# Optimization experiments

Hardware: AMD Instinct MI355X
Metric: run time of the kernel (lower is better)

## Reference

```python
import jax, jax.numpy as jnp
import numpy as np

B, S, H, V, NH, FF, M, NL = 16, 512, 256, 8000, 4, 512, 64, 2
BETA, THR, ALPHA = 0.9, 1.0, 2.0  # snn.Leaky defaults: beta=0.9, threshold=1.0, ATan surrogate alpha=2


@jax.custom_vjp
def spike(u):
    return (u > 0).astype(u.dtype)

def _spike_fwd(u):
    return (u > 0).astype(u.dtype), u

def _spike_bwd(u, g):
    # snntorch ATan surrogate gradient
    return (g * (ALPHA / 2.0) / (1.0 + (jnp.pi * u * ALPHA / 2.0) ** 2),)

spike.defvjp(_spike_fwd, _spike_bwd)


def layer_norm(x, g, b):
    m = x.mean(-1, keepdims=True)
    v = ((x - m) ** 2).mean(-1, keepdims=True)
    return (x - m) / jnp.sqrt(v + 1e-5) * g + b


def mha(x, wqkv, bqkv, wo, bo):
    Bx, Sx, Hx = x.shape
    hd = Hx // NH
    qkv = x @ wqkv.T + bqkv
    q, k, v = jnp.split(qkv, 3, axis=-1)
    sp = lambda t: t.reshape(Bx, Sx, NH, hd).transpose(0, 2, 1, 3)
    q, k, v = sp(q), sp(k), sp(v)
    att = jax.nn.softmax(jnp.einsum('bhqd,bhkd->bhqk', q, k) / (float(hd) ** 0.5), axis=-1)
    o = jnp.einsum('bhqk,bhkd->bhqd', att, v).transpose(0, 2, 1, 3).reshape(Bx, Sx, Hx)
    return o @ wo.T + bo


def spiking_worker(x, w, b):
    # batched projection for all timesteps, then a single-pass LIF scan
    proj = x @ w.T + b  # [B,S,H]

    def step(mem, xt):
        reset = spike(mem - THR)              # spike detected from previous membrane
        mem = BETA * mem + xt - reset * THR   # subtract-reset mechanism
        return mem, spike(mem - THR)

    mem0 = jnp.zeros((x.shape[0], x.shape[2]), x.dtype)
    _, spks = jax.lax.scan(step, mem0, jnp.swapaxes(proj, 0, 1))
    return jnp.swapaxes(spks, 0, 1)  # [B,S,H]


def _forward(input_ids, embed, pos, qkv_w, qkv_b, out_w, out_b, ln1_g, ln1_b,
             ff1_w, ff1_b, ff2_w, ff2_b, ln2_g, ln2_b,
             log_w, log_b, mat_w, mat_b, conv_w, conv_b,
             read_w, read_b, memory, head_w, head_b):
    x = embed[input_ids] + pos[:, :input_ids.shape[1], :]
    for i in range(NL):  # post-norm TransformerEncoderLayer x2, gelu, eval mode
        x = layer_norm(x + mha(x, qkv_w[i], qkv_b[i], out_w[i], out_b[i]), ln1_g[i], ln1_b[i])
        h = jax.nn.gelu(x @ ff1_w[i].T + ff1_b[i], approximate=False) @ ff2_w[i].T + ff2_b[i]
        x = layer_norm(x + h, ln2_g[i], ln2_b[i])
    plan = x
    logico = spiking_worker(plan, log_w, log_b)
    matem = spiking_worker(plan, mat_w, mat_b)
    ling = jax.lax.conv_general_dilated(
        jnp.swapaxes(plan, 1, 2), conv_w, (1,), [(1, 1)],
        dimension_numbers=('NCH', 'OIH', 'NCH')) + conv_b[None, :, None]
    ling = jnp.swapaxes(ling, 1, 2)
    combined = jnp.concatenate([logico, matem, ling, plan], axis=-1)  # [B,S,4H]
    plan_mean = plan.mean(axis=1)                                      # [B,H]
    read_weights = jax.nn.softmax(plan_mean @ read_w.T + read_b, axis=-1)
    memory_read = read_weights @ memory                                # [B,H]
    logits = combined @ head_w.T + head_b                              # [B,S,V]
    return logits, memory_read


def setup_inputs() -> dict:
    key = jax.random.key(0)
    ks = iter(jax.random.split(key, 32))
    sc = 0.02
    rn = lambda shape, s=sc: jax.random.normal(next(ks), shape, jnp.float32) * s
    inp = {
        'input_ids': jax.random.randint(next(ks), (B, S), 0, V),
        'embed': rn((V, H), 1.0),
        'pos': rn((1, 512, H), 1.0),
        'qkv_w': rn((NL, 3 * H, H)), 'qkv_b': rn((NL, 3 * H)),
        'out_w': rn((NL, H, H)), 'out_b': rn((NL, H)),
        'ln1_g': jnp.ones((NL, H), jnp.float32), 'ln1_b': jnp.zeros((NL, H), jnp.float32),
        'ff1_w': rn((NL, FF, H)), 'ff1_b': rn((NL, FF)),
        'ff2_w': rn((NL, H, FF)), 'ff2_b': rn((NL, H)),
        'ln2_g': jnp.ones((NL, H), jnp.float32), 'ln2_b': jnp.zeros((NL, H), jnp.float32),
        'log_w': rn((H, H)), 'log_b': rn((H,)),
        'mat_w': rn((H, H)), 'mat_b': rn((H,)),
        'conv_w': rn((H, H, 3)), 'conv_b': rn((H,)),
        'read_w': rn((M, H)), 'read_b': rn((M,)),
        'memory': rn((M, H), 1.0),
        'head_w': rn((V, 4 * H)), 'head_b': rn((V,)),
    }
    return inp


def reference(input_ids, embed, pos, qkv_w, qkv_b, out_w, out_b, ln1_g, ln1_b,
              ff1_w, ff1_b, ff2_w, ff2_b, ln2_g, ln2_b,
              log_w, log_b, mat_w, mat_b, conv_w, conv_b,
              read_w, read_b, memory, head_w, head_b):
    return _forward(input_ids, embed, pos, qkv_w, qkv_b, out_w, out_b, ln1_g, ln1_b,
                    ff1_w, ff1_b, ff2_w, ff2_b, ln2_g, ln2_b,
                    log_w, log_b, mat_w, mat_b, conv_w, conv_b,
                    read_w, read_b, memory, head_w, head_b)
```

## Files before the change

### kernel.cpp

```cpp
#include <hip/hip_runtime.h>
#include <hip/hip_bf16.h>

constexpr int Bc = 16, Sc = 512, Hc = 256, Vc = 8000, NHc = 4, HDc = 64;
constexpr int FFc = 512, Mc = 64;
constexpr int ROWS = Bc * Sc;
constexpr int CH = 4 * Hc;
constexpr int NT2 = CH / 32;

typedef __attribute__((ext_vector_type(4))) float f32x4v;
typedef __attribute__((ext_vector_type(8))) short short8v;
typedef __attribute__((ext_vector_type(4))) short short4v;
typedef __hip_bfloat16 bf16;

__device__ inline void split3(float x, bf16& h, bf16& m, bf16& l) {
    h = __float2bfloat16(x);
    const float r = x - __bfloat162float(h);
    m = __float2bfloat16(r);
    const float r2 = r - __bfloat162float(m);
    l = __float2bfloat16(r2);
}

__device__ __forceinline__ void split_range(const float* __restrict__ in,
                                            bf16* __restrict__ h, bf16* __restrict__ m,
                                            bf16* __restrict__ l, int blk, int t) {
    const size_t i = ((size_t)blk * 256 + t) * 4;
    const float4 v = *(const float4*)&in[i];
    split3(v.x, h[i + 0], m[i + 0], l[i + 0]);
    split3(v.y, h[i + 1], m[i + 1], l[i + 1]);
    split3(v.z, h[i + 2], m[i + 2], l[i + 2]);
    split3(v.w, h[i + 3], m[i + 3], l[i + 3]);
}

__global__ __launch_bounds__(256) void k_prep(
    const float* __restrict__ qkv_w, const float* __restrict__ out_w,
    const float* __restrict__ ff1_w, const float* __restrict__ ff2_w,
    const float* __restrict__ log_w, const float* __restrict__ mat_w,
    const float* __restrict__ conv_w, const float* __restrict__ head_w,
    const float* __restrict__ log_b, const float* __restrict__ mat_b,
    bf16* qkvwh, bf16* qkvwm, bf16* qkvwl,
    bf16* outwh, bf16* outwm, bf16* outwl,
    bf16* ff1wh, bf16* ff1wm, bf16* ff1wl,
    bf16* ff2wh, bf16* ff2wm, bf16* ff2wl,
    bf16* lmwh, bf16* lmwm, bf16* lmwl,
    bf16* w2h, bf16* w2m, bf16* w2l,
    bf16* hwb, float* lmb) {
    const int blk = blockIdx.x;
    const int t = threadIdx.x;
    if (blk < 384) {
        split_range(qkv_w, qkvwh, qkvwm, qkvwl, blk, t);
    } else if (blk < 512) {
        split_range(out_w, outwh, outwm, outwl, blk - 384, t);
    } else if (blk < 768) {
        split_range(ff1_w, ff1wh, ff1wm, ff1wl, blk - 512, t);
    } else if (blk < 1024) {
        split_range(ff2_w, ff2wh, ff2wm, ff2wl, blk - 768, t);
    } else if (blk < 1088) {
        split_range(log_w, lmwh, lmwm, lmwl, blk - 1024, t);
    } else if (blk < 1152) {
        split_range(mat_w, lmwh + 65536, lmwm + 65536, lmwl + 65536, blk - 1088, t);
    } else if (blk < 1920) {
        const int idx = (blk - 1152) * 256 + t;
        const int o = idx / 768, rem = idx % 768;
        const int k = rem >> 8, i = rem & 255;
        split3(conv_w[(size_t)o * 768 + i * 3 + k], w2h[idx], w2m[idx], w2l[idx]);
    } else if (blk < 9920) {
        const size_t i = ((size_t)(blk - 1920) * 256 + t) * 4;
        const float4 v = *(const float4*)&head_w[i];
        bf16 b0 = __float2bfloat16(v.x), b1 = __float2bfloat16(v.y);
        bf16 b2 = __float2bfloat16(v.z), b3 = __float2bfloat16(v.w);
        short4v sv;
        sv[0] = *(const short*)&b0; sv[1] = *(const short*)&b1;
        sv[2] = *(const short*)&b2; sv[3] = *(const short*)&b3;
        *(short4v*)(hwb + i) = sv;
    } else {
        lmb[t] = log_b[t];
        lmb[256 + t] = mat_b[t];
    }
}

__global__ __launch_bounds__(256) void k_embed(const int* __restrict__ ids,
                                               const float* __restrict__ emb,
                                               const float* __restrict__ pos,
                                               float* __restrict__ x,
                                               bf16* __restrict__ xh, bf16* __restrict__ xm,
                                               bf16* __restrict__ xl) {
    const int r = blockIdx.x;
    const int h = threadIdx.x;
    const int s = r & (Sc - 1);
    const int id = ids[r];
    const float v = emb[(size_t)id * Hc + h] + pos[(size_t)s * Hc + h];
    const size_t o = (size_t)r * Hc + h;
    x[o] = v;
    split3(v, xh[o], xm[o], xl[o]);
}

template <int EPI, int OUTS, int BN>
__global__ __launch_bounds__(256) void k_bg3(
    const bf16* __restrict__ Ah, const bf16* __restrict__ Am, const bf16* __restrict__ Al,
    const bf16* __restrict__ Bh, const bf16* __restrict__ Bm, const bf16* __restrict__ Bl,
    const float* __restrict__ bias, float* __restrict__ C,
    bf16* __restrict__ Oh, bf16* __restrict__ Om, bf16* __restrict__ Ol,
    int K, int lda, int ldb, int ldc,
    long zA2, long zA1, long zB2, long zB1, long zC2, long zC1) {
    constexpr int NF = BN / 32;
    __shared__ bf16 As[3][128 * 32];
    __shared__ bf16 Bs[3][BN * 32];
    const int z = blockIdx.z, z2 = z >> 2, z1 = z & 3;
    const size_t aoff = (size_t)z2 * zA2 + (size_t)z1 * zA1;
    const size_t boff = (size_t)z2 * zB2 + (size_t)z1 * zB1;
    const size_t coff = (size_t)z2 * zC2 + (size_t)z1 * zC1;
    const int t = threadIdx.x;
    const int tm = blockIdx.x * 128, tn = blockIdx.y * BN;
    const int w = t >> 6, l = t & 63;
    const int wr = w >> 1, wc = w & 1;
    const bf16* Ap[3] = {Ah, Am, Al};
    const bf16* Bp[3] = {Bh, Bm, Bl};
    f32x4v acc[4][NF];
    const f32x4v zero = {0.f, 0.f, 0.f, 0.f};
#pragma unroll
    for (int i = 0; i < 4; ++i)
#pragma unroll
        for (int j = 0; j < NF; ++j) acc[i][j] = zero;

    for (int kt = 0; kt < K; kt += 32) {
#pragma unroll
        for (int p = 0; p < 3; ++p) {
#pragma unroll
            for (int j = 0; j < 2; ++j) {
                const int c = j * 256 + t;
                const int row = c >> 2, kc = c & 3;
                const int skc = kc ^ ((row >> 1) & 3);
                const bf16* ga = Ap[p] + aoff + (size_t)(tm + row) * lda + kt + skc * 8;
                __builtin_amdgcn_global_load_lds((const __attribute__((address_space(1))) void*)ga,
                                                 (__attribute__((address_space(3))) void*)(&As[p][0] + c * 8),
                                                 16, 0, 0);
            }
            if (BN == 128) {
#pragma unroll
                for (int j = 0; j < 2; ++j) {
                    const int c = j * 256 + t;
                    const int row = c >> 2, kc = c & 3;
                    const int skc = kc ^ ((row >> 1) & 3);
                    const bf16* gb = Bp[p] + boff + (size_t)(tn + row) * ldb + kt + skc * 8;
                    __builtin_amdgcn_global_load_lds((const __attribute__((address_space(1))) void*)gb,
                                                     (__attribute__((address_space(3))) void*)(&Bs[p][0] + c * 8),
                                                     16, 0, 0);
                }
            } else {
                const int c = t;
                const int row = c >> 2, kc = c & 3;
                const int skc = kc ^ ((row >> 1) & 3);
                const bf16* gb = Bp[p] + boff + (size_t)(tn + row) * ldb + kt + skc * 8;
                __builtin_amdgcn_global_load_lds((const __attribute__((address_space(1))) void*)gb,
                                                 (__attribute__((address_space(3))) void*)(&Bs[p][0] + c * 8),
                                                 16, 0, 0);
            }
        }
        __syncthreads();
        const int lr = l & 15, lkc = l >> 4;
        short8v af[3][4], bfr[3][NF];
#pragma unroll
        for (int p = 0; p < 3; ++p)
#pragma unroll
            for (int m = 0; m < 4; ++m) {
                const int row = wr * 64 + m * 16 + lr;
                const int sc = lkc ^ ((row >> 1) & 3);
                af[p][m] = *(const short8v*)(&As[p][0] + row * 32 + sc * 8);
            }
#pragma unroll
        for (int p = 0; p < 3; ++p)
#pragma unroll
            for (int n = 0; n < NF; ++n) {
                const int row = wc * (BN / 2) + n * 16 + lr;
                const int sc = lkc ^ ((row >> 1) & 3);
                bfr[p][n] = *(const short8v*)(&Bs[p][0] + row * 32 + sc * 8);
            }
#pragma unroll
        for (int m = 0; m < 4; ++m)
#pragma unroll
            for (int n = 0; n < NF; ++n)
                acc[m][n] = __builtin_amdgcn_mfma_f32_16x16x32_bf16(af[0][m], bfr[0][n], acc[m][n], 0, 0, 0);
#pragma unroll
        for (int m = 0; m < 4; ++m)
#pragma unroll
            for (int n = 0; n < NF; ++n)
                acc[m][n] = __builtin_amdgcn_mfma_f32_16x16x32_bf16(af[0][m], bfr[1][n], acc[m][n], 0, 0, 0);
#pragma unroll
        for (int m = 0; m < 4; ++m)
#pragma unroll
            for (int n = 0; n < NF; ++n)
                acc[m][n] = __builtin_amdgcn_mfma_f32_16x16x32_bf16(af[1][m], bfr[0][n], acc[m][n], 0, 0, 0);
#pragma unroll
        for (int m = 0; m < 4; ++m)
#pragma unroll
            for (int n = 0; n < NF; ++n)
                acc[m][n] = __builtin_amdgcn_mfma_f32_16x16x32_bf16(af[0][m], bfr[2][n], acc[m][n], 0, 0, 0);
#pragma unroll
        for (int m = 0; m < 4; ++m)
#pragma unroll
            for (int n = 0; n < NF; ++n)
                acc[m][n] = __builtin_amdgcn_mfma_f32_16x16x32_bf16(af[2][m], bfr[0][n], acc[m][n], 0, 0, 0);
#pragma unroll
        for (int m = 0; m < 4; ++m)
#pragma unroll
            for (int n = 0; n < NF; ++n)
                acc[m][n] = __builtin_amdgcn_mfma_f32_16x16x32_bf16(af[1][m], bfr[1][n], acc[m][n], 0, 0, 0);
        __syncthreads();
    }
    const int lr = l & 15, lq = (l >> 4) * 4;
#pragma unroll
    for (int n = 0; n < NF; ++n) {
        const int col = tn + wc * (BN / 2) + n * 16 + lr;
        const float bv = (EPI == 0 || EPI == 1) ? bias[col] : 0.0f;
#pragma unroll
        for (int m = 0; m < 4; ++m) {
            const int rbase = tm + wr * 64 + m * 16 + lq;
#pragma unroll
            for (int j = 0; j < 4; ++j) {
                float v = acc[m][n][j];
                if (EPI == 0) v += bv;
                if (EPI == 1) { v += bv; v = 0.5f * v * (1.0f + erff(v / 1.41421356237309515f)); }
                const size_t o = coff + (size_t)(rbase + j) * ldc + col;
                if (OUTS == 0) C[o] = v;
                else if (OUTS == 3) ((bf16*)C)[o] = __float2bfloat16(v);
                else split3(v, Oh[o], Om[o], Ol[o]);
            }
        }
    }
}

__global__ __launch_bounds__(256) void k_vt(const bf16* __restrict__ qh,
                                            const bf16* __restrict__ qm,
                                            const bf16* __restrict__ ql,
                                            bf16* __restrict__ vh, bf16* __restrict__ vm,
                                            bf16* __restrict__ vl) {
    __shared__ bf16 tile[64][72];
    const int sblk = blockIdx.x;
    const int z = blockIdx.y;
    const int b = z >> 2, h = z & 3;
    const int t = threadIdx.x;
    const int sr = t >> 2, c16 = (t & 3) * 16;
    const bf16* qp[3] = {qh, qm, ql};
    bf16* vp[3] = {vh, vm, vl};
    for (int p = 0; p < 3; ++p) {
        const bf16* src = qp[p] + (size_t)(b * Sc + sblk * 64 + sr) * 768 + 512 + h * 64 + c16;
        *(short8v*)&tile[sr][c16] = *(const short8v*)src;
        *(short8v*)&tile[sr][c16 + 8] = *(const short8v*)(src + 8);
        __syncthreads();
        bf16 out[16];
#pragma unroll
        for (int i = 0; i < 16; ++i) out[i] = tile[c16 + i][sr];
        bf16* dst = vp[p] + (size_t)(z * 64 + sr) * Sc + sblk * 64 + c16;
        *(short8v*)dst = *(short8v*)&out[0];
        *(short8v*)(dst + 8) = *(short8v*)&out[8];
        __syncthreads();
    }
}

#define S_PASS(QA, KB)                                                                     \
    _Pragma("unroll") for (int m = 0; m < 2; ++m) _Pragma("unroll") for (int ks = 0; ks < 2; ++ks) \
        sa[m] = __builtin_amdgcn_mfma_f32_16x16x32_bf16(QA[m][ks], KB[ks], sa[m], 0, 0, 0);
#define PV_PASS(PA, VB)                                                                    \
    _Pragma("unroll") for (int m = 0; m < 2; ++m) _Pragma("unroll") for (int ks = 0; ks < 2; ++ks) \
        oa[m] = __builtin_amdgcn_mfma_f32_16x16x32_bf16(PA[m][ks], VB[ks], oa[m], 0, 0, 0);

__global__ __launch_bounds__(512) void k_attn(
    const bf16* __restrict__ qph, const bf16* __restrict__ qpm, const bf16* __restrict__ qpl,
    const bf16* __restrict__ vth, const bf16* __restrict__ vtm, const bf16* __restrict__ vtl,
    bf16* __restrict__ oh, bf16* __restrict__ om, bf16* __restrict__ ol) {
    extern __shared__ char smem[];
    float* S = (float*)smem;
    bf16* KV0 = (bf16*)(smem + 131072);
    bf16* KV1 = KV0 + 4096;
    bf16* KV2 = KV1 + 4096;
    const int qc = blockIdx.x, z = blockIdx.y;
    const int b = z >> 2, hh = z & 3;
    const int t = threadIdx.x;
    const int w = t >> 6, lane = t & 63;
    const int lr = lane & 15, lkc = lane >> 4;
    const int qg = w >> 2, kg = w & 3;
    const int r8 = t >> 3, c8 = t & 7;
    const f32x4v zero = {0.f, 0.f, 0.f, 0.f};

    short8v qf0[2][2], qf1[2][2], qf2[2][2];
#pragma unroll
    for (int m = 0; m < 2; ++m)
#pragma unroll
        for (int ks = 0; ks < 2; ++ks) {
            const size_t rbase = (size_t)(b * 512 + qc * 64 + qg * 32 + m * 16 + lr) * 768 + hh * 64 + ks * 32 + lkc * 8;
            qf0[m][ks] = *(const short8v*)(qph + rbase);
            qf1[m][ks] = *(const short8v*)(qpm + rbase);
            qf2[m][ks] = *(const short8v*)(qpl + rbase);
        }

    {
        const size_t srow = (size_t)(b * 512 + 0 * 64 + r8) * 768 + 256 + hh * 64 + (c8 ^ (r8 & 7)) * 8;
        __builtin_amdgcn_global_load_lds((const __attribute__((address_space(1))) void*)(qph + srow),
                                         (__attribute__((address_space(3))) void*)(KV0 + r8 * 64 + c8 * 8), 16, 0, 0);
        __builtin_amdgcn_global_load_lds((const __attribute__((address_space(1))) void*)(qpm + srow),
                                         (__attribute__((address_space(3))) void*)(KV1 + r8 * 64 + c8 * 8), 16, 0, 0);
        __builtin_amdgcn_global_load_lds((const __attribute__((address_space(1))) void*)(qpl + srow),
                                         (__attribute__((address_space(3))) void*)(KV2 + r8 * 64 + c8 * 8), 16, 0, 0);
    }

    for (int kv = 0; kv < 8; ++kv) {
        __syncthreads();
        short8v kb0[2], kb1[2], kb2[2];
#pragma unroll
        for (int ks = 0; ks < 2; ++ks) {
            const int row = kg * 16 + lr;
            const int sc = (ks * 4 + lkc) ^ (row & 7);
            kb0[ks] = *(const short8v*)(KV0 + row * 64 + sc * 8);
            kb1[ks] = *(const short8v*)(KV1 + row * 64 + sc * 8);
            kb2[ks] = *(const short8v*)(KV2 + row * 64 + sc * 8);
        }
        __syncthreads();
        if (kv < 7) {
            const size_t srow = (size_t)(b * 512 + (kv + 1) * 64 + r8) * 768 + 256 + hh * 64 + (c8 ^ (r8 & 7)) * 8;
            __builtin_amdgcn_global_load_lds((const __attribute__((address_space(1))) void*)(qph + srow),
                                             (__attribute__((address_space(3))) void*)(KV0 + r8 * 64 + c8 * 8), 16, 0, 0);
            __builtin_amdgcn_global_load_lds((const __attribute__((address_space(1))) void*)(qpm + srow),
                                             (__attribute__((address_space(3))) void*)(KV1 + r8 * 64 + c8 * 8), 16, 0, 0);
            __builtin_amdgcn_global_load_lds((const __attribute__((address_space(1))) void*)(qpl + srow),
                                             (__attribute__((address_space(3))) void*)(KV2 + r8 * 64 + c8 * 8), 16, 0, 0);
        } else {
            const size_t srow = (size_t)(z * 64 + r8) * 512 + 0 * 64 + (c8 ^ (r8 & 7)) * 8;
            __builtin_amdgcn_global_load_lds((const __attribute__((address_space(1))) void*)(vth + srow),
                                             (__attribute__((address_space(3))) void*)(KV0 + r8 * 64 + c8 * 8), 16, 0, 0);
            __builtin_amdgcn_global_load_lds((const __attribute__((address_space(1))) void*)(vtm + srow),
                                             (__attribute__((address_space(3))) void*)(KV1 + r8 * 64 + c8 * 8), 16, 0, 0);
            __builtin_amdgcn_global_load_lds((const __attribute__((address_space(1))) void*)(vtl + srow),
                                             (__attribute__((address_space(3))) void*)(KV2 + r8 * 64 + c8 * 8), 16, 0, 0);
        }
        f32x4v sa[2] = {zero, zero};
        S_PASS(qf0, kb0) S_PASS(qf0, kb1) S_PASS(qf1, kb0)
        S_PASS(qf0, kb2) S_PASS(qf2, kb0) S_PASS(qf1, kb1)
#pragma unroll
        for (int m = 0; m < 2; ++m)
#pragma unroll
            for (int j = 0; j < 4; ++j) {
                const int row = qg * 32 + m * 16 + (lane >> 4) * 4 + j;
                const int col = kv * 64 + kg * 16 + lr;
                const int chunk = (col >> 2) ^ (row & 7);
                *(float*)((char*)S + row * 2048 + chunk * 16 + (col & 3) * 4) = sa[m][j] * 0.125f;
            }
    }
    __syncthreads();

    for (int r = 0; r < 8; ++r) {
        const int row = w * 8 + r;
        char* rowp = (char*)S + row * 2048;
        const int sw = row & 7;
        float4 x0 = *(float4*)(rowp + ((2 * lane) ^ sw) * 16);
        float4 x1 = *(float4*)(rowp + ((2 * lane + 1) ^ sw) * 16);
        float mx = fmaxf(fmaxf(fmaxf(x0.x, x0.y), fmaxf(x0.z, x0.w)),
                         fmaxf(fmaxf(x1.x, x1.y), fmaxf(x1.z, x1.w)));
#pragma unroll
        for (int d = 1; d < 64; d <<= 1) mx = fmaxf(mx, __shfl_xor(mx, d));
        const float e0 = expf(x0.x - mx), e1 = expf(x0.y - mx), e2 = expf(x0.z - mx), e3 = expf(x0.w - mx);
        const float e4 = expf(x1.x - mx), e5 = expf(x1.y - mx), e6 = expf(x1.z - mx), e7 = expf(x1.w - mx);
        float sm = ((e0 + e1) + (e2 + e3)) + ((e4 + e5) + (e6 + e7));
#pragma unroll
        for (int d = 1; d < 64; d <<= 1) sm += __shfl_xor(sm, d);
        x0.x = e0 / sm; x0.y = e1 / sm; x0.z = e2 / sm; x0.w = e3 / sm;
        x1.x = e4 / sm; x1.y = e5 / sm; x1.z = e6 / sm; x1.w = e7 / sm;
        *(float4*)(rowp + ((2 * lane) ^ sw) * 16) = x0;
        *(float4*)(rowp + ((2 * lane + 1) ^ sw) * 16) = x1;
    }
    __syncthreads();

    f32x4v oa[2] = {zero, zero};
    for (int kv = 0; kv < 8; ++kv) {
        if (kv > 0) __syncthreads();
        short8v vb0[2], vb1[2], vb2[2];
#pragma unroll
        for (int ks = 0; ks < 2; ++ks) {
            const int rowd = kg * 16 + lr;
            const int sc = (ks * 4 + lkc) ^ (rowd & 7);
            vb0[ks] = *(const short8v*)(KV0 + rowd * 64 + sc * 8);
            vb1[ks] = *(const short8v*)(KV1 + rowd * 64 + sc * 8);
            vb2[ks] = *(const short8v*)(KV2 + rowd * 64 + sc * 8);
        }
        __syncthreads();
        if (kv < 7) {
            const size_t srow = (size_t)(z * 64 + r8) * 512 + (kv + 1) * 64 + (c8 ^ (r8 & 7)) * 8;
            __builtin_amdgcn_global_load_lds((const __attribute__((address_space(1))) void*)(vth + srow),
                                             (__attribute__((address_space(3))) void*)(KV0 + r8 * 64 + c8 * 8), 16, 0, 0);
            __builtin_amdgcn_global_load_lds((const __attribute__((address_space(1))) void*)(vtm + srow),
                                             (__attribute__((address_space(3))) void*)(KV1 + r8 * 64 + c8 * 8), 16, 0, 0);
            __builtin_amdgcn_global_load_lds((const __attribute__((address_space(1))) void*)(vtl + srow),
                                             (__attribute__((address_space(3))) void*)(KV2 + r8 * 64 + c8 * 8), 16, 0, 0);
        }
        short8v pah[2][2], pam[2][2], pal[2][2];
#pragma unroll
        for (int m = 0; m < 2; ++m)
#pragma unroll
            for (int ks = 0; ks < 2; ++ks) {
                const int row = qg * 32 + m * 16 + lr;
                const int c0 = kv * 16 + ks * 8 + lkc * 2;
                char* rp = (char*)S + row * 2048;
                const float4 y0 = *(const float4*)(rp + (c0 ^ (row & 7)) * 16);
                const float4 y1 = *(const float4*)(rp + ((c0 + 1) ^ (row & 7)) * 16);
                const float yy[8] = {y0.x, y0.y, y0.z, y0.w, y1.x, y1.y, y1.z, y1.w};
                short8v hv, mv, lv;
#pragma unroll
                for (int i = 0; i < 8; ++i) {
                    bf16 a, bq, c;
                    split3(yy[i], a, bq, c);
                    hv[i] = *(const short*)&a; mv[i] = *(const short*)&bq; lv[i] = *(const short*)&c;
                }
                pah[m][ks] = hv; pam[m][ks] = mv; pal[m][ks] = lv;
            }
        PV_PASS(pah, vb0) PV_PASS(pah, vb1) PV_PASS(pam, vb0)
        PV_PASS(pah, vb2) PV_PASS(pal, vb0) PV_PASS(pam, vb1)
    }
#pragma unroll
    for (int m = 0; m < 2; ++m)
#pragma unroll
        for (int j = 0; j < 4; ++j) {
            const int grow = b * 512 + qc * 64 + qg * 32 + m * 16 + (lane >> 4) * 4 + j;
            const int col = hh * 64 + kg * 16 + lr;
            const size_t o = (size_t)grow * 256 + col;
            split3(oa[m][j], oh[o], om[o], ol[o]);
        }
}

__global__ __launch_bounds__(256) void k_add_ln(float* __restrict__ x,
                                                const float* __restrict__ res,
                                                const float* __restrict__ g,
                                                const float* __restrict__ b,
                                                bf16* __restrict__ xh, bf16* __restrict__ xm,
                                                bf16* __restrict__ xl,
                                                bf16* __restrict__ comb) {
    const int w = threadIdx.x >> 6, lane = threadIdx.x & 63;
    const size_t row = (size_t)blockIdx.x * 4 + w;
    float v[4];
#pragma unroll
    for (int j = 0; j < 4; ++j) {
        const int e = lane + j * 64;
        v[j] = x[row * Hc + e] + res[row * Hc + e];
    }
    float a = v[0] + v[2];
    float bb = v[1] + v[3];
    float c = a + bb;
#pragma unroll
    for (int d = 32; d >= 1; d >>= 1) c += __shfl_xor(c, d);
    const float mean = c * (1.0f / 256.0f);
    float dd[4], sq[4];
#pragma unroll
    for (int j = 0; j < 4; ++j) {
        dd[j] = v[j] - mean;
        sq[j] = dd[j] * dd[j];
        asm volatile("" : "+v"(sq[j]));
    }
    float a2 = sq[0] + sq[2];
    float b2 = sq[1] + sq[3];
    float c2 = a2 + b2;
#pragma unroll
    for (int d = 32; d >= 1; d >>= 1) c2 += __shfl_xor(c2, d);
    const float var = c2 * (1.0f / 256.0f);
    const float rstd = sqrtf(var + 1e-5f);
#pragma unroll
    for (int j = 0; j < 4; ++j) {
        const int e = lane + j * 64;
        const float out = dd[j] / rstd * g[e] + b[e];
        const size_t o = row * Hc + e;
        x[o] = out;
        split3(out, xh[o], xm[o], xl[o]);
        if (comb != nullptr) comb[row * CH + 768 + e] = __float2bfloat16(out);
    }
}

__global__ __launch_bounds__(256) void k_lif2(const float* __restrict__ lm,
                                              bf16* __restrict__ comb) {
    const int b = blockIdx.x;
    const int half = blockIdx.y;
    const int h = threadIdx.x;
    const float* p = lm + (size_t)b * Sc * 512 + half * 256 + h;
    bf16* o = comb + (size_t)b * Sc * CH + half * 256 + h;
    float mem = 0.0f;
    for (int s0 = 0; s0 < Sc; s0 += 8) {
        float xs[8];
#pragma unroll
        for (int q = 0; q < 8; ++q) xs[q] = p[(size_t)(s0 + q) * 512];
#pragma unroll
        for (int q = 0; q < 8; ++q) {
            const float reset = (mem > 1.0f) ? 1.0f : 0.0f;
            float t1 = 0.9f * mem;
            asm volatile("" : "+v"(t1));
            float t2 = t1 + xs[q];
            asm volatile("" : "+v"(t2));
            mem = t2 - reset;
            o[(size_t)(s0 + q) * CH] = __float2bfloat16((mem > 1.0f) ? 1.0f : 0.0f);
        }
    }
}

__global__ __launch_bounds__(256) void k_aext3(const bf16* __restrict__ xh,
                                               const bf16* __restrict__ xm,
                                               const bf16* __restrict__ xl,
                                               bf16* __restrict__ aeh, bf16* __restrict__ aem,
                                               bf16* __restrict__ ael) {
    const int idx = blockIdx.x * 256 + threadIdx.x;
    const int row = idx / 192, c4 = idx % 192;
    const int c = c4 * 4;
    const int k = c >> 8, i = c & 255;
    const int b = row >> 9, s = row & 511;
    const int ss = s + k - 1;
    const size_t dst = (size_t)row * 768 + c;
    if (ss >= 0 && ss < Sc) {
        const size_t src = (size_t)(b * Sc + ss) * Hc + i;
        *(short4v*)(aeh + dst) = *(const short4v*)(xh + src);
        *(short4v*)(aem + dst) = *(const short4v*)(xm + src);
        *(short4v*)(ael + dst) = *(const short4v*)(xl + src);
    } else {
        const short4v z = {0, 0, 0, 0};
        *(short4v*)(aeh + dst) = z;
        *(short4v*)(aem + dst) = z;
        *(short4v*)(ael + dst) = z;
    }
}

__device__ __forceinline__ void stageA32(const bf16* __restrict__ g, int rbase,
                                         bf16* lbase, int kt, int t) {
#pragma unroll
    for (int q = 0; q < 2; ++q) {
        const int f = q * 256 + t;
        const int rowt = f >> 2, chunk = f & 3;
        const int sch = chunk ^ ((rowt >> 1) & 3);
        const bf16* gp = g + (size_t)(rbase + rowt) * CH + kt * 32 + sch * 8;
        __builtin_amdgcn_global_load_lds((const __attribute__((address_space(1))) void*)gp,
                                         (__attribute__((address_space(3))) void*)(lbase + rowt * 32 + chunk * 8),
                                         16, 0, 0);
    }
}
__device__ __forceinline__ void stageB32(const bf16* __restrict__ g, int rbase, int rmax,
                                         bf16* lbase, int kt, int t) {
#pragma unroll
    for (int q = 0; q < 4; ++q) {
        const int f = q * 256 + t;
        const int rowt = f >> 2, chunk = f & 3;
        const int sch = chunk ^ ((rowt >> 1) & 3);
        int grow = rbase + rowt;
        if (grow > rmax) grow = rmax;
        const bf16* gp = g + (size_t)grow * CH + kt * 32 + sch * 8;
        __builtin_amdgcn_global_load_lds((const __attribute__((address_space(1))) void*)gp,
                                         (__attribute__((address_space(3))) void*)(lbase + rowt * 32 + chunk * 8),
                                         16, 0, 0);
    }
}

__global__ __launch_bounds__(256, 2) void k_head8(const bf16* __restrict__ Abf,
                                                  const bf16* __restrict__ Bbf,
                                                  const float* __restrict__ bias,
                                                  float* __restrict__ C) {
    __shared__ bf16 LA[2][128 * 32];
    __shared__ bf16 LB[2][256 * 32];
    const int t = threadIdx.x;
    const int w = t >> 6, lane = t & 63;
    const int wn = w;
    const int tm = blockIdx.x * 128, tn = blockIdx.y * 256;
    const int lr = lane & 15, lkc = lane >> 4;

    f32x4v acc[8][4];
    const f32x4v zero = {0.f, 0.f, 0.f, 0.f};
#pragma unroll
    for (int m = 0; m < 8; ++m)
#pragma unroll
        for (int n = 0; n < 4; ++n) acc[m][n] = zero;

    stageA32(Abf, tm, LA[0], 0, t);
    stageB32(Bbf, tn, Vc - 1, LB[0], 0, t);
    stageA32(Abf, tm, LA[1], 1, t);
    asm volatile("s_waitcnt vmcnt(2)" ::: "memory");
    __builtin_amdgcn_s_barrier();
    __builtin_amdgcn_sched_barrier(0);

    for (int kt = 0; kt < NT2; ++kt) {
        bf16* la = LA[kt & 1];
        bf16* lb = LB[kt & 1];
        bf16* lbN = LB[(kt + 1) & 1];
        short8v a[8], b[4];
#pragma unroll
        for (int m = 0; m < 8; ++m) {
            const int row = m * 16 + lr;
            const int sc = lkc ^ ((row >> 1) & 3);
            a[m] = *(const short8v*)(la + row * 32 + sc * 8);
        }
#pragma unroll
        for (int n = 0; n < 4; ++n) {
            const int row = wn * 64 + n * 16 + lr;
            const int sc = lkc ^ ((row >> 1) & 3);
            b[n] = *(const short8v*)(lb + row * 32 + sc * 8);
        }
        if (kt + 1 < NT2) stageB32(Bbf, tn, Vc - 1, lbN, kt + 1, t);
        __builtin_amdgcn_s_barrier();
        __builtin_amdgcn_sched_barrier(0);
        __builtin_amdgcn_s_setprio(1);
#pragma unroll
        for (int m = 0; m < 8; ++m)
#pragma unroll
            for (int n = 0; n < 2; ++n)
                acc[m][n] = __builtin_amdgcn_mfma_f32_16x16x32_bf16(a[m], b[n], acc[m][n], 0, 0, 0);
        __builtin_amdgcn_s_setprio(0);
        __builtin_amdgcn_s_barrier();
        __builtin_amdgcn_sched_barrier(0);
        if (kt + 2 < NT2) stageA32(Abf, tm, la, kt + 2, t);
        __builtin_amdgcn_s_setprio(1);
#pragma unroll
        for (int m = 0; m < 8; ++m)
#pragma unroll
            for (int n = 2; n < 4; ++n)
                acc[m][n] = __builtin_amdgcn_mfma_f32_16x16x32_bf16(a[m], b[n], acc[m][n], 0, 0, 0);
        __builtin_amdgcn_s_setprio(0);
        if (kt + 2 < NT2) asm volatile("s_waitcnt vmcnt(2)" ::: "memory");
        else              asm volatile("s_waitcnt vmcnt(0)" ::: "memory");
        __builtin_amdgcn_s_barrier();
        __builtin_amdgcn_sched_barrier(0);
    }
    const int lq = (lane >> 4) * 4;
#pragma unroll
    for (int n = 0; n < 4; ++n) {
        const int col = tn + wn * 64 + n * 16 + lr;
        if (col >= Vc) continue;
        const float bv = bias[col];
#pragma unroll
        for (int m = 0; m < 8; ++m) {
            const int rbase = tm + m * 16 + lq;
#pragma unroll
            for (int j = 0; j < 4; ++j)
                C[(size_t)(rbase + j) * Vc + col] = acc[m][n][j] + bv;
        }
    }
}

__global__ __launch_bounds__(256) void k_pmean(const float* __restrict__ plan, float* __restrict__ pm2) {
    const int b = blockIdx.x, c = blockIdx.y;
    const int h = threadIdx.x;
    const float* p = plan + ((size_t)(b * Sc + c * 64)) * Hc + h;
    float s = 0.0f;
    for (int i = 0; i < 64; ++i) s += p[(size_t)i * Hc];
    pm2[((size_t)b * 8 + c) * Hc + h] = s;
}

__global__ __launch_bounds__(256) void k_memread(const float* __restrict__ pm2,
                                                 const float* __restrict__ rw,
                                                 const float* __restrict__ rb,
                                                 const float* __restrict__ memm,
                                                 float* __restrict__ out) {
    const int b = blockIdx.x;
    const int t = threadIdx.x;
    __shared__ float pms[256];
    __shared__ float lg[64];
    __shared__ float sm[64];
    float v = 0.0f;
    for (int c = 0; c < 8; ++c) v += pm2[((size_t)b * 8 + c) * Hc + t];
    pms[t] = v * (1.0f / 512.0f);
    __syncthreads();
    if (t < 64) {
        float s = rb[t];
        const float* wrow = rw + (size_t)t * Hc;
        for (int i = 0; i < Hc; ++i) s = fmaf(wrow[i], pms[i], s);
        lg[t] = s;
    }
    __syncthreads();
    if (t == 0) {
        float mx = lg[0];
        for (int i = 1; i < 64; ++i) mx = fmaxf(mx, lg[i]);
        float ssum = 0.0f;
        for (int i = 0; i < 64; ++i) { const float e = expf(lg[i] - mx); sm[i] = e; ssum += e; }
        for (int i = 0; i < 64; ++i) sm[i] /= ssum;
    }
    __syncthreads();
    float s = 0.0f;
    for (int m = 0; m < 64; ++m) s = fmaf(sm[m], memm[(size_t)m * Hc + t], s);
    out[(size_t)b * Hc + t] = s;
}

extern "C" void kernel_launch(void* const* d_in, const int* in_sizes, int n_in,
                              void* d_out, int out_size, void* d_ws, size_t ws_size,
                              hipStream_t stream) {
    const int*   ids    = (const int*)  d_in[0];
    const float* embed  = (const float*)d_in[1];
    const float* pos    = (const float*)d_in[2];
    const float* qkv_w  = (const float*)d_in[3];
    const float* qkv_b  = (const float*)d_in[4];
    const float* out_w  = (const float*)d_in[5];
    const float* out_b  = (const float*)d_in[6];
    const float* ln1_g  = (const float*)d_in[7];
    const float* ln1_b  = (const float*)d_in[8];
    const float* ff1_w  = (const float*)d_in[9];
    const float* ff1_b  = (const float*)d_in[10];
    const float* ff2_w  = (const float*)d_in[11];
    const float* ff2_b  = (const float*)d_in[12];
    const float* ln2_g  = (const float*)d_in[13];
    const float* ln2_b  = (const float*)d_in[14];
    const float* log_w  = (const float*)d_in[15];
    const float* log_b  = (const float*)d_in[16];
    const float* mat_w  = (const float*)d_in[17];
    const float* mat_b  = (const float*)d_in[18];
    const float* conv_w = (const float*)d_in[19];
    const float* conv_b = (const float*)d_in[20];
    const float* read_w = (const float*)d_in[21];
    const float* read_b = (const float*)d_in[22];
    const float* memory = (const float*)d_in[23];
    const float* head_w = (const float*)d_in[24];
    const float* head_b = (const float*)d_in[25];

    char* wsb = (char*)d_ws;
    const size_t MB = 1ull << 20;
    float* X    = (float*)(wsb + 0);
    bf16*  XH   = (bf16*)(wsb + 8 * MB);
    bf16*  XM   = (bf16*)(wsb + 12 * MB);
    bf16*  XL   = (bf16*)(wsb + 16 * MB);
    float* RES  = (float*)(wsb + 20 * MB);
    bf16*  QPH  = (bf16*)(wsb + 28 * MB);
    bf16*  QPM  = (bf16*)(wsb + 40 * MB);
    bf16*  QPL  = (bf16*)(wsb + 52 * MB);
    bf16*  OH   = (bf16*)(wsb + 64 * MB);
    bf16*  OM   = (bf16*)(wsb + 68 * MB);
    bf16*  OL   = (bf16*)(wsb + 72 * MB);
    bf16*  VTH  = (bf16*)(wsb + 76 * MB);
    bf16*  VTM  = (bf16*)(wsb + 80 * MB);
    bf16*  VTL  = (bf16*)(wsb + 84 * MB);
    bf16*  H1H  = (bf16*)(wsb + 88 * MB);
    bf16*  H1M  = (bf16*)(wsb + 96 * MB);
    bf16*  H1L  = (bf16*)(wsb + 104 * MB);
    float* LOGMAT = (float*)(wsb + 76 * MB);
    bf16*  AEH  = (bf16*)(wsb + 92 * MB);
    bf16*  AEM  = (bf16*)(wsb + 104 * MB);
    bf16*  AEL  = (bf16*)(wsb + 116 * MB);
    bf16*  COMB = (bf16*)(wsb + 128 * MB);
    bf16*  HWB  = (bf16*)(wsb + 144 * MB);
    bf16*  WP   = (bf16*)(wsb + 160 * MB);
    float* PM2  = (float*)(wsb + 64 * MB);

    float* logits = (float*)d_out;
    float* mread  = logits + (size_t)ROWS * Vc;

    bf16* qkvwh = WP;             bf16* qkvwm = qkvwh + 393216; bf16* qkvwl = qkvwm + 393216;
    bf16* outwh = qkvwl + 393216; bf16* outwm = outwh + 131072; bf16* outwl = outwm + 131072;
    bf16* ff1wh = outwl + 131072; bf16* ff1wm = ff1wh + 262144; bf16* ff1wl = ff1wm + 262144;
    bf16* ff2wh = ff1wl + 262144; bf16* ff2wm = ff2wh + 262144; bf16* ff2wl = ff2wm + 262144;
    bf16* lmwh  = ff2wl + 262144; bf16* lmwm  = lmwh + 131072;  bf16* lmwl  = lmwm + 131072;
    bf16* w2h   = lmwl + 131072;  bf16* w2m   = w2h + 196608;   bf16* w2l   = w2m + 196608;
    float* LMB  = (float*)(w2l + 196608);

    hipFuncSetAttribute((const void*)k_attn, hipFuncAttributeMaxDynamicSharedMemorySize, 155648);

    k_prep<<<dim3(9921), 256, 0, stream>>>(
        qkv_w, out_w, ff1_w, ff2_w, log_w, mat_w, conv_w, head_w, log_b, mat_b,
        qkvwh, qkvwm, qkvwl, outwh, outwm, outwl, ff1wh, ff1wm, ff1wl,
        ff2wh, ff2wm, ff2wl, lmwh, lmwm, lmwl, w2h, w2m, w2l, HWB, LMB);

    k_embed<<<dim3(ROWS), 256, 0, stream>>>(ids, embed, pos, X, XH, XM, XL);
    for (int l = 0; l < 2; ++l) {
        k_bg3<0, 1, 128><<<dim3(64, 6, 1), 256, 0, stream>>>(
            XH, XM, XL,
            qkvwh + (size_t)l * 196608, qkvwm + (size_t)l * 196608, qkvwl + (size_t)l * 196608,
            qkv_b + l * 768, nullptr, QPH, QPM, QPL,
            256, 256, 256, 768, 0, 0, 0, 0, 0, 0);
        k_vt<<<dim3(8, 64), 256, 0, stream>>>(QPH, QPM, QPL, VTH, VTM, VTL);
        k_attn<<<dim3(8, 64), 512, 155648, stream>>>(QPH, QPM, QPL, VTH, VTM, VTL, OH, OM, OL);
        k_bg3<0, 0, 64><<<dim3(64, 4, 1), 256, 0, stream>>>(
            OH, OM, OL,
            outwh + (size_t)l * 65536, outwm + (size_t)l * 65536, outwl + (size_t)l * 65536,
            out_b + l * 256, RES, nullptr, nullptr, nullptr,
            256, 256, 256, 256, 0, 0, 0, 0, 0, 0);
        k_add_ln<<<dim3(ROWS / 4), 256, 0, stream>>>(X, RES, ln1_g + l * 256, ln1_b + l * 256,
                                                     XH, XM, XL, nullptr);
        k_bg3<1, 1, 128><<<dim3(64, 4, 1), 256, 0, stream>>>(
            XH, XM, XL,
            ff1wh + (size_t)l * 131072, ff1wm + (size_t)l * 131072, ff1wl + (size_t)l * 131072,
            ff1_b + l * 512, nullptr, H1H, H1M, H1L,
            256, 256, 256, 512, 0, 0, 0, 0, 0, 0);
        k_bg3<0, 0, 64><<<dim3(64, 4, 1), 256, 0, stream>>>(
            H1H, H1M, H1L,
            ff2wh + (size_t)l * 131072, ff2wm + (size_t)l * 131072, ff2wl + (size_t)l * 131072,
            ff2_b + l * 256, RES, nullptr, nullptr, nullptr,
            512, 512, 512, 256, 0, 0, 0, 0, 0, 0);
        k_add_ln<<<dim3(ROWS / 4), 256, 0, stream>>>(X, RES, ln2_g + l * 256, ln2_b + l * 256,
                                                     XH, XM, XL, (l == 1) ? COMB : nullptr);
    }
    k_bg3<0, 0, 128><<<dim3(64, 4, 1), 256, 0, stream>>>(
        XH, XM, XL, lmwh, lmwm, lmwl, LMB, LOGMAT, nullptr, nullptr, nullptr,
        256, 256, 256, 512, 0, 0, 0, 0, 0, 0);
    k_aext3<<<dim3(6144), 256, 0, stream>>>(XH, XM, XL, AEH, AEM, AEL);
    k_lif2<<<dim3(Bc, 2), 256, 0, stream>>>(LOGMAT, COMB);
    k_bg3<0, 3, 64><<<dim3(64, 4, 1), 256, 0, stream>>>(
        AEH, AEM, AEL, w2h, w2m, w2l, conv_b, (float*)(COMB + 512), nullptr, nullptr, nullptr,
        768, 768, 768, CH, 0, 0, 0, 0, 0, 0);
    k_head8<<<dim3(64, 32), 256, 0, stream>>>(COMB, HWB, head_b, logits);
    k_pmean<<<dim3(Bc, 8), 256, 0, stream>>>(X, PM2);
    k_memread<<<dim3(Bc), 256, 0, stream>>>(PM2, read_w, read_b, memory, mread);
}
```

Before: 720.8 us.

## Fuse conv im2col into GEMM loads, vectorize embed, batch vt transposes

Removes the separate im2col kernel (k_aext3) that materialized a 3x-expanded activation in three bf16 planes. The conv GEMM now computes shifted source addresses on the fly and points out-of-range halo rows at a small zero buffer. This saves roughly 36MB of writes plus the matching re-reads. The embed kernel is vectorized to four rows per block using float4/short4 accesses, and k_vt loads all three precision planes before a single sync instead of syncing per plane. The address computation in the GEMM load loop adds some integer work per load.

```diff
diff --git a/kernel.cpp b/kernel.cpp
--- a/kernel.cpp
+++ b/kernel.cpp
@@ -43,7 +43,7 @@
     bf16* ff2wh, bf16* ff2wm, bf16* ff2wl,
     bf16* lmwh, bf16* lmwm, bf16* lmwl,
     bf16* w2h, bf16* w2m, bf16* w2l,
-    bf16* hwb, float* lmb) {
+    bf16* hwb, float* lmb, bf16* zb) {
     const int blk = blockIdx.x;
     const int t = threadIdx.x;
     if (blk < 384) {
@@ -75,6 +75,7 @@
     } else {
         lmb[t] = log_b[t];
         lmb[256 + t] = mat_b[t];
+        if (t < 64) ((short*)zb)[t] = 0;
     }
 }
 
@@ -84,24 +85,37 @@
                                                float* __restrict__ x,
                                                bf16* __restrict__ xh, bf16* __restrict__ xm,
                                                bf16* __restrict__ xl) {
-    const int r = blockIdx.x;
-    const int h = threadIdx.x;
+    const int w = threadIdx.x >> 6, lane = threadIdx.x & 63;
+    const int r = blockIdx.x * 4 + w;
     const int s = r & (Sc - 1);
     const int id = ids[r];
-    const float v = emb[(size_t)id * Hc + h] + pos[(size_t)s * Hc + h];
-    const size_t o = (size_t)r * Hc + h;
-    x[o] = v;
-    split3(v, xh[o], xm[o], xl[o]);
-}
-
-template <int EPI, int OUTS, int BN>
+    const int e0 = lane * 4;
+    const float4 ev = *(const float4*)&emb[(size_t)id * Hc + e0];
+    const float4 pv = *(const float4*)&pos[(size_t)s * Hc + e0];
+    const float v[4] = {ev.x + pv.x, ev.y + pv.y, ev.z + pv.z, ev.w + pv.w};
+    const size_t o = (size_t)r * Hc + e0;
+    *(float4*)(x + o) = *(const float4*)&v[0];
+    short4v sh, sm, sl;
+#pragma unroll
+    for (int j = 0; j < 4; ++j) {
+        bf16 a, b, c;
+        split3(v[j], a, b, c);
+        sh[j] = *(const short*)&a; sm[j] = *(const short*)&b; sl[j] = *(const short*)&c;
+    }
+    *(short4v*)(xh + o) = sh;
+    *(short4v*)(xm + o) = sm;
+    *(short4v*)(xl + o) = sl;
+}
+
+template <int EPI, int OUTS, int BN, int HALO = 0>
 __global__ __launch_bounds__(256) void k_bg3(
     const bf16* __restrict__ Ah, const bf16* __restrict__ Am, const bf16* __restrict__ Al,
     const bf16* __restrict__ Bh, const bf16* __restrict__ Bm, const bf16* __restrict__ Bl,
     const float* __restrict__ bias, float* __restrict__ C,
     bf16* __restrict__ Oh, bf16* __restrict__ Om, bf16* __restrict__ Ol,
     int K, int lda, int ldb, int ldc,
-    long zA2, long zA1, long zB2, long zB1, long zC2, long zC1) {
+    long zA2, long zA1, long zB2, long zB1, long zC2, long zC1,
+    const bf16* __restrict__ zb) {
     constexpr int NF = BN / 32;
     __shared__ bf16 As[3][128 * 32];
     __shared__ bf16 Bs[3][BN * 32];
@@ -130,7 +144,17 @@
                 const int c = j * 256 + t;
                 const int row = c >> 2, kc = c & 3;
                 const int skc = kc ^ ((row >> 1) & 3);
-                const bf16* ga = Ap[p] + aoff + (size_t)(tm + row) * lda + kt + skc * 8;
+                const bf16* ga;
+                if (HALO) {
+                    const int kk = kt + skc * 8;
+                    const int dk = kk >> 8, ii = kk & 255;
+                    const int grow = tm + row;
+                    const int bb = grow >> 9, s = grow & 511;
+                    const int ss = s + dk - 1;
+                    ga = (ss >= 0 && ss < Sc) ? (Ap[p] + ((size_t)(bb * Sc + ss) * Hc + ii)) : zb;
+                } else {
+                    ga = Ap[p] + aoff + (size_t)(tm + row) * lda + kt + skc * 8;
+                }
                 __builtin_amdgcn_global_load_lds((const __attribute__((address_space(1))) void*)ga,
                                                  (__attribute__((address_space(3))) void*)(&As[p][0] + c * 8),
                                                  16, 0, 0);
@@ -234,7 +258,7 @@
                                             const bf16* __restrict__ ql,
                                             bf16* __restrict__ vh, bf16* __restrict__ vm,
                                             bf16* __restrict__ vl) {
-    __shared__ bf16 tile[64][72];
+    __shared__ bf16 tile[3][64][72];
     const int sblk = blockIdx.x;
     const int z = blockIdx.y;
     const int b = z >> 2, h = z & 3;
@@ -242,18 +266,21 @@
     const int sr = t >> 2, c16 = (t & 3) * 16;
     const bf16* qp[3] = {qh, qm, ql};
     bf16* vp[3] = {vh, vm, vl};
+#pragma unroll
     for (int p = 0; p < 3; ++p) {
         const bf16* src = qp[p] + (size_t)(b * Sc + sblk * 64 + sr) * 768 + 512 + h * 64 + c16;
-        *(short8v*)&tile[sr][c16] = *(const short8v*)src;
-        *(short8v*)&tile[sr][c16 + 8] = *(const short8v*)(src + 8);
-        __syncthreads();
+        *(short8v*)&tile[p][sr][c16] = *(const short8v*)src;
+        *(short8v*)&tile[p][sr][c16 + 8] = *(const short8v*)(src + 8);
+    }
+    __syncthreads();
+#pragma unroll
+    for (int p = 0; p < 3; ++p) {
         bf16 out[16];
 #pragma unroll
-        for (int i = 0; i < 16; ++i) out[i] = tile[c16 + i][sr];
+        for (int i = 0; i < 16; ++i) out[i] = tile[p][c16 + i][sr];
         bf16* dst = vp[p] + (size_t)(z * 64 + sr) * Sc + sblk * 64 + c16;
         *(short8v*)dst = *(short8v*)&out[0];
         *(short8v*)(dst + 8) = *(short8v*)&out[8];
-        __syncthreads();
     }
 }
 
@@ -493,31 +520,6 @@
             mem = t2 - reset;
             o[(size_t)(s0 + q) * CH] = __float2bfloat16((mem > 1.0f) ? 1.0f : 0.0f);
         }
-    }
-}
-
-__global__ __launch_bounds__(256) void k_aext3(const bf16* __restrict__ xh,
-                                               const bf16* __restrict__ xm,
-                                               const bf16* __restrict__ xl,
-                                               bf16* __restrict__ aeh, bf16* __restrict__ aem,
-                                               bf16* __restrict__ ael) {
-    const int idx = blockIdx.x * 256 + threadIdx.x;
-    const int row = idx / 192, c4 = idx % 192;
-    const int c = c4 * 4;
-    const int k = c >> 8, i = c & 255;
-    const int b = row >> 9, s = row & 511;
-    const int ss = s + k - 1;
-    const size_t dst = (size_t)row * 768 + c;
-    if (ss >= 0 && ss < Sc) {
-        const size_t src = (size_t)(b * Sc + ss) * Hc + i;
-        *(short4v*)(aeh + dst) = *(const short4v*)(xh + src);
-        *(short4v*)(aem + dst) = *(const short4v*)(xm + src);
-        *(short4v*)(ael + dst) = *(const short4v*)(xl + src);
-    } else {
-        const short4v z = {0, 0, 0, 0};
-        *(short4v*)(aeh + dst) = z;
-        *(short4v*)(aem + dst) = z;
-        *(short4v*)(ael + dst) = z;
     }
 }
 
@@ -727,9 +729,6 @@
     bf16*  H1M  = (bf16*)(wsb + 96 * MB);
     bf16*  H1L  = (bf16*)(wsb + 104 * MB);
     float* LOGMAT = (float*)(wsb + 76 * MB);
-    bf16*  AEH  = (bf16*)(wsb + 92 * MB);
-    bf16*  AEM  = (bf16*)(wsb + 104 * MB);
-    bf16*  AEL  = (bf16*)(wsb + 116 * MB);
     bf16*  COMB = (bf16*)(wsb + 128 * MB);
     bf16*  HWB  = (bf16*)(wsb + 144 * MB);
     bf16*  WP   = (bf16*)(wsb + 160 * MB);
@@ -745,51 +744,51 @@
     bf16* lmwh  = ff2wl + 262144; bf16* lmwm  = lmwh + 131072;  bf16* lmwl  = lmwm + 131072;
     bf16* w2h   = lmwl + 131072;  bf16* w2m   = w2h + 196608;   bf16* w2l   = w2m + 196608;
     float* LMB  = (float*)(w2l + 196608);
+    bf16*  ZB   = (bf16*)((char*)LMB + 2048);
 
     hipFuncSetAttribute((const void*)k_attn, hipFuncAttributeMaxDynamicSharedMemorySize, 155648);
 
     k_prep<<<dim3(9921), 256, 0, stream>>>(
         qkv_w, out_w, ff1_w, ff2_w, log_w, mat_w, conv_w, head_w, log_b, mat_b,
         qkvwh, qkvwm, qkvwl, outwh, outwm, outwl, ff1wh, ff1wm, ff1wl,
-        ff2wh, ff2wm, ff2wl, lmwh, lmwm, lmwl, w2h, w2m, w2l, HWB, LMB);
-
-    k_embed<<<dim3(ROWS), 256, 0, stream>>>(ids, embed, pos, X, XH, XM, XL);
+        ff2wh, ff2wm, ff2wl, lmwh, lmwm, lmwl, w2h, w2m, w2l, HWB, LMB, ZB);
+
+    k_embed<<<dim3(ROWS / 4), 256, 0, stream>>>(ids, embed, pos, X, XH, XM, XL);
     for (int l = 0; l < 2; ++l) {
         k_bg3<0, 1, 128><<<dim3(64, 6, 1), 256, 0, stream>>>(
             XH, XM, XL,
             qkvwh + (size_t)l * 196608, qkvwm + (size_t)l * 196608, qkvwl + (size_t)l * 196608,
             qkv_b + l * 768, nullptr, QPH, QPM, QPL,
-            256, 256, 256, 768, 0, 0, 0, 0, 0, 0);
+            256, 256, 256, 768, 0, 0, 0, 0, 0, 0, nullptr);
         k_vt<<<dim3(8, 64), 256, 0, stream>>>(QPH, QPM, QPL, VTH, VTM, VTL);
         k_attn<<<dim3(8, 64), 512, 155648, stream>>>(QPH, QPM, QPL, VTH, VTM, VTL, OH, OM, OL);
         k_bg3<0, 0, 64><<<dim3(64, 4, 1), 256, 0, stream>>>(
             OH, OM, OL,
             outwh + (size_t)l * 65536, outwm + (size_t)l * 65536, outwl + (size_t)l * 65536,
             out_b + l * 256, RES, nullptr, nullptr, nullptr,
-            256, 256, 256, 256, 0, 0, 0, 0, 0, 0);
+            256, 256, 256, 256, 0, 0, 0, 0, 0, 0, nullptr);
         k_add_ln<<<dim3(ROWS / 4), 256, 0, stream>>>(X, RES, ln1_g + l * 256, ln1_b + l * 256,
                                                      XH, XM, XL, nullptr);
         k_bg3<1, 1, 128><<<dim3(64, 4, 1), 256, 0, stream>>>(
             XH, XM, XL,
             ff1wh + (size_t)l * 131072, ff1wm + (size_t)l * 131072, ff1wl + (size_t)l * 131072,
             ff1_b + l * 512, nullptr, H1H, H1M, H1L,
-            256, 256, 256, 512, 0, 0, 0, 0, 0, 0);
+            256, 256, 256, 512, 0, 0, 0, 0, 0, 0, nullptr);
         k_bg3<0, 0, 64><<<dim3(64, 4, 1), 256, 0, stream>>>(
             H1H, H1M, H1L,
             ff2wh + (size_t)l * 131072, ff2wm + (size_t)l * 131072, ff2wl + (size_t)l * 131072,
             ff2_b + l * 256, RES, nullptr, nullptr, nullptr,
-            512, 512, 512, 256, 0, 0, 0, 0, 0, 0);
+            512, 512, 512, 256, 0, 0, 0, 0, 0, 0, nullptr);
         k_add_ln<<<dim3(ROWS / 4), 256, 0, stream>>>(X, RES, ln2_g + l * 256, ln2_b + l * 256,
                                                      XH, XM, XL, (l == 1) ? COMB : nullptr);
     }
     k_bg3<0, 0, 128><<<dim3(64, 4, 1), 256, 0, stream>>>(
         XH, XM, XL, lmwh, lmwm, lmwl, LMB, LOGMAT, nullptr, nullptr, nullptr,
-        256, 256, 256, 512, 0, 0, 0, 0, 0, 0);
-    k_aext3<<<dim3(6144), 256, 0, stream>>>(XH, XM, XL, AEH, AEM, AEL);
+        256, 256, 256, 512, 0, 0, 0, 0, 0, 0, nullptr);
     k_lif2<<<dim3(Bc, 2), 256, 0, stream>>>(LOGMAT, COMB);
-    k_bg3<0, 3, 64><<<dim3(64, 4, 1), 256, 0, stream>>>(
-        AEH, AEM, AEL, w2h, w2m, w2l, conv_b, (float*)(COMB + 512), nullptr, nullptr, nullptr,
-        768, 768, 768, CH, 0, 0, 0, 0, 0, 0);
+    k_bg3<0, 3, 64, 1><<<dim3(64, 4, 1), 256, 0, stream>>>(
+        XH, XM, XL, w2h, w2m, w2l, conv_b, (float*)(COMB + 512), nullptr, nullptr, nullptr,
+        768, 256, 768, CH, 0, 0, 0, 0, 0, 0, ZB);
     k_head8<<<dim3(64, 32), 256, 0, stream>>>(COMB, HWB, head_b, logits);
     k_pmean<<<dim3(Bc, 8), 256, 0, stream>>>(X, PM2);
     k_memread<<<dim3(Bc), 256, 0, stream>>>(PM2, read_w, read_b, memory, mread);
```

New measurement: 705.6 us (median of 2 runs). 1.02x faster.
